# Optimization experiments

Measured on AMD Instinct MI355X. Metric: run time of the kernel, lower is better.

## Reference

```python
import jax, jax.numpy as jnp
import numpy as np

B = 4096
HASH_BITS = 128
TEACHER_DIM = 768
TEMPERATURE = 0.2
CONTRASTIVE_W = 1.0
DISTILL_W = 0.5
QUANT_W = 0.01


def _l2_normalize(x, eps=1e-12):
    # matches torch F.normalize(dim=-1)
    n = jnp.sqrt(jnp.sum(x * x, axis=-1, keepdims=True))
    return x / jnp.maximum(n, eps)


def setup_inputs() -> dict:
    key = jax.random.key(0)
    k1, k2, k3, k4 = jax.random.split(key, 4)
    logits = jax.random.normal(k1, (B, HASH_BITS), dtype=jnp.float32)
    # binary {-1,+1} codes as in the module contract
    hash_codes = jnp.sign(jax.random.normal(k2, (B, HASH_BITS), dtype=jnp.float32))
    hash_codes = jnp.where(hash_codes == 0, 1.0, hash_codes)
    teacher_embed = jax.random.normal(k3, (B, TEACHER_DIM), dtype=jnp.float32)
    # sparse random positives plus self-positives (guarantees each row nonempty)
    rand_pos = jax.random.uniform(k4, (B, B)) < 0.002
    eye = jnp.eye(B, dtype=bool)
    positive_mask = rand_pos | eye
    return {
        "logits": logits,
        "hash_codes": hash_codes,
        "teacher_embed": teacher_embed,
        "positive_mask": positive_mask,
    }


def reference(logits, hash_codes, teacher_embed, positive_mask):
    teacher = _l2_normalize(teacher_embed)

    # ---- contrastive (vectorized form of the per-row python loop) ----
    ln = _l2_normalize(logits)
    sim = (ln @ ln.T) / TEMPERATURE  # [B, B]
    eye = jnp.eye(sim.shape[0], dtype=bool)
    sim_masked = jnp.where(eye, -jnp.inf, sim)
    # per-row stable logsumexp over self-masked similarities
    log_denom = jax.nn.logsumexp(sim_masked, axis=1)  # [B]
    pm = positive_mask.astype(sim.dtype)
    cnt = pm.sum(axis=1)  # [B]
    pos_mean = (sim * pm).sum(axis=1) / jnp.maximum(cnt, 1.0)
    has_pos = cnt > 0
    per_row = jnp.where(has_pos, -pos_mean + log_denom, 0.0)
    num_pos = jnp.maximum(has_pos.sum(), 1)
    loss_cont = per_row.sum() / num_pos.astype(sim.dtype)

    # ---- distillation: hash similarity vs teacher similarity MSE ----
    hash_sim = (hash_codes @ hash_codes.T) / hash_codes.shape[-1]
    teacher_sim = teacher @ teacher.T
    loss_distill = jnp.mean((hash_sim - teacher_sim) ** 2)

    # ---- quantization: push |logits| toward 1 ----
    loss_quant = jnp.mean(jnp.abs(jnp.abs(logits) - 1.0))

    total = (
        CONTRASTIVE_W * loss_cont
        + DISTILL_W * loss_distill
        + QUANT_W * loss_quant
    )
    return total
```

## Files before the change

### kernel.cpp

```cpp
#include <hip/hip_runtime.h>


typedef __bf16 bf16x8 __attribute__((ext_vector_type(8)));
typedef float f32x4 __attribute__((ext_vector_type(4)));

__device__ __forceinline__ unsigned short f2bf(float f) {
  union { float f; unsigned int u; } v; v.f = f;
  unsigned int u = v.u;
  return (unsigned short)((u + 0x7FFFu + ((u >> 16) & 1u)) >> 16);
}

__global__ __launch_bounds__(256) void prep(const float* __restrict__ logits,
                                            const float* __restrict__ hash,
                                            const float* __restrict__ teacher,
                                            unsigned short* __restrict__ P,
                                            unsigned char* __restrict__ QT,
                                            float* __restrict__ qpart,
                                            float* __restrict__ rowexp,
                                            float* __restrict__ possum,
                                            float* __restrict__ cntw,
                                            float* __restrict__ dtot) {
  __shared__ float rnt[16];
  __shared__ unsigned char QL[16 * 897];
  const int t = threadIdx.x, wave = t >> 6, lane = t & 63;
  const int r0 = (int)blockIdx.x * 16;

#pragma unroll
  for (int rr = 0; rr < 4; ++rr) {
    const int rl = wave * 4 + rr, r = r0 + rl;
    float ss = 0.f;
#pragma unroll
    for (int i = 0; i < 12; ++i) {
      const float v = teacher[(size_t)r * 768 + i * 64 + lane];
      ss += v * v;
    }
    const float l0 = logits[(size_t)r * 128 + lane];
    const float l1 = logits[(size_t)r * 128 + 64 + lane];
    float ssl = l0 * l0 + l1 * l1;
    float qv = fabsf(fabsf(l0) - 1.f) + fabsf(fabsf(l1) - 1.f);
#pragma unroll
    for (int off = 1; off < 64; off <<= 1) {
      ss += __shfl_xor(ss, off, 64);
      ssl += __shfl_xor(ssl, off, 64);
      qv += __shfl_xor(qv, off, 64);
    }
    const float rnl = 1.f / fmaxf(sqrtf(ssl), 1e-12f);
    P[(size_t)r * 128 + lane] = f2bf(l0 * rnl);
    P[(size_t)r * 128 + 64 + lane] = f2bf(l1 * rnl);
    if (lane == 0) {
      rnt[rl] = 11.313708498984761f / fmaxf(sqrtf(ss), 1e-12f);
      qpart[r] = qv;
    }
  }
  if (t < 16) { rowexp[r0 + t] = 0.f; possum[r0 + t] = 0.f; cntw[r0 + t] = 0.f; }
  if (blockIdx.x == 0 && t == 0) *dtot = 0.f;
  __syncthreads();

#pragma unroll
  for (int it = 0; it < 4; ++it) {
    const int task = it * 256 + t;
    if (task < 896) {
      const int r = task / 56, cb = task % 56;
      const int r_g = r0 + r;
      unsigned char* dst = &QL[r * 897 + cb * 16];
      if (cb < 8) {
        const float4 v0 = *(const float4*)&hash[(size_t)r_g * 128 + cb * 16];
        const float4 v1 = *(const float4*)&hash[(size_t)r_g * 128 + cb * 16 + 4];
        const float4 v2 = *(const float4*)&hash[(size_t)r_g * 128 + cb * 16 + 8];
        const float4 v3 = *(const float4*)&hash[(size_t)r_g * 128 + cb * 16 + 12];
        const float vv[16] = {v0.x, v0.y, v0.z, v0.w, v1.x, v1.y, v1.z, v1.w,
                              v2.x, v2.y, v2.z, v2.w, v3.x, v3.y, v3.z, v3.w};
#pragma unroll
        for (int k = 0; k < 16; ++k) dst[k] = vv[k] >= 0.f ? 0x38 : 0xB8;
      } else {
        const float sc = rnt[r];
        const int c0 = cb * 16 - 128;
        const float4 v0 = *(const float4*)&teacher[(size_t)r_g * 768 + c0];
        const float4 v1 = *(const float4*)&teacher[(size_t)r_g * 768 + c0 + 4];
        const float4 v2 = *(const float4*)&teacher[(size_t)r_g * 768 + c0 + 8];
        const float4 v3 = *(const float4*)&teacher[(size_t)r_g * 768 + c0 + 12];
        const float vv[16] = {v0.x, v0.y, v0.z, v0.w, v1.x, v1.y, v1.z, v1.w,
                              v2.x, v2.y, v2.z, v2.w, v3.x, v3.y, v3.z, v3.w};
#pragma unroll
        for (int k = 0; k < 16; ++k) {
          const int p8 = __builtin_amdgcn_cvt_pk_fp8_f32(vv[k] * sc, vv[k] * sc,
                                                         0, false);
          dst[k] = (unsigned char)(p8 & 0xFF);
        }
      }
    }
  }
  __syncthreads();

#pragma unroll
  for (int i = 0; i < 4; ++i) {
    const int c = t + 256 * i;
    if (c < 896) {
      unsigned char buf[16];
#pragma unroll
      for (int j = 0; j < 16; ++j) buf[j] = QL[j * 897 + c];
      *(uint4*)&QT[(size_t)c * 4096 + r0] = *(uint4*)buf;
    }
  }
}

#define STAGE_GEN(GA, GB, PITCH)                                               \
  {                                                                            \
    _Pragma("unroll") for (int it = 0; it < 4; ++it) {                         \
      const int task = it * 256 + t;                                           \
      const int row = task >> 3;                                               \
      const int c16 = (task & 7) ^ (row & 7);                                  \
      const unsigned char* gpA = (GA) + (size_t)row * (PITCH) + c16 * 16;      \
      __builtin_amdgcn_global_load_lds(                                        \
          (const __attribute__((address_space(1))) void*)gpA,                  \
          (__attribute__((address_space(3))) void*)&SB[it * 4096 + wave * 1024],\
          16, 0, 0);                                                           \
      if (offdiag) {                                                           \
        const unsigned char* gpB = (GB) + (size_t)row * (PITCH) + c16 * 16;    \
        __builtin_amdgcn_global_load_lds(                                      \
            (const __attribute__((address_space(1))) void*)gpB,                \
            (__attribute__((address_space(3)))                                 \
                 void*)&SB[16384 + it * 4096 + wave * 1024],                   \
            16, 0, 0);                                                         \
      }                                                                        \
    }                                                                          \
  }

#define MFMA_B()                                                               \
  {                                                                            \
    _Pragma("unroll") for (int ks = 0; ks < 2; ++ks) {                         \
      const int ph = ((ks * 4 + qd) ^ (l15 & 7)) * 16;                         \
      bf16x8 af[4], bfr[4];                                                    \
      _Pragma("unroll") for (int rt = 0; rt < 4; ++rt)                         \
          af[rt] = *(const bf16x8*)&SB[(wy * 64 + rt * 16 + l15) * 128 + ph];  \
      _Pragma("unroll") for (int ct = 0; ct < 4; ++ct)                         \
          bfr[ct] = *(const bf16x8*)&SB[boffB +                                \
                                        (wx * 64 + ct * 16 + l15) * 128 + ph]; \
      _Pragma("unroll") for (int rt = 0; rt < 4; ++rt)                         \
          _Pragma("unroll") for (int ct = 0; ct < 4; ++ct) acc[rt][ct] =       \
          __builtin_amdgcn_mfma_f32_16x16x32_bf16(af[rt], bfr[ct],             \
                                                  acc[rt][ct], 0, 0, 0);       \
    }                                                                          \
  }

#define MFMA_Q()                                                               \
  {                                                                            \
    _Pragma("unroll") for (int ks = 0; ks < 4; ++ks) {                         \
      const int g0 = ks * 4 + qd;                                              \
      const int ph = ((g0 >> 1) ^ (l15 & 7)) * 16 + (g0 & 1) * 8;              \
      long af[4], bfr[4];                                                      \
      _Pragma("unroll") for (int rt = 0; rt < 4; ++rt)                         \
          af[rt] = *(const long*)&SB[(wy * 64 + rt * 16 + l15) * 128 + ph];    \
      _Pragma("unroll") for (int ct = 0; ct < 4; ++ct)                         \
          bfr[ct] = *(const long*)&SB[boffB +                                  \
                                      (wx * 64 + ct * 16 + l15) * 128 + ph];   \
      _Pragma("unroll") for (int rt = 0; rt < 4; ++rt)                         \
          _Pragma("unroll") for (int ct = 0; ct < 4; ++ct) acc[rt][ct] =       \
          __builtin_amdgcn_mfma_f32_16x16x32_fp8_fp8(af[rt], bfr[ct],          \
                                                     acc[rt][ct], 0, 0, 0);    \
    }                                                                          \
  }

__global__ __launch_bounds__(256, 3) void mega(const unsigned short* __restrict__ P,
                                               const unsigned char* __restrict__ QT,
                                               const void* __restrict__ mask,
                                               float* __restrict__ rowexp,
                                               float* __restrict__ possum,
                                               float* __restrict__ cntw,
                                               float* __restrict__ dtot) {
  __shared__ __align__(16) unsigned char SB[32768];
  __shared__ float redrow[128][2], red4[4];

  const int t = threadIdx.x;
  const int wave = t >> 6, lane = t & 63;
  const int qd = lane >> 4, l15 = lane & 15;
  const int wy = wave >> 1, wx = wave & 1;
  const int b = (int)blockIdx.x;

  f32x4 acc[4][4];
#pragma unroll
  for (int rt = 0; rt < 4; ++rt)
#pragma unroll
    for (int ct = 0; ct < 4; ++ct) acc[rt][ct] = {0.f, 0.f, 0.f, 0.f};

  if (b < 28) {
    int I = 0, rem = b;
    while (rem >= 7 - I) { rem -= 7 - I; ++I; }
    const int J = I + rem;
    const bool offdiag = (I != J);
    const int boffB = offdiag ? 16384 : 0;
    const unsigned char* QA = QT + (size_t)I * 128 * 4096;
    const unsigned char* QB = QT + (size_t)J * 128 * 4096;
    for (int kc = 0; kc < 32; ++kc) {
      __syncthreads();
      STAGE_GEN(QA + kc * 128, QB + kc * 128, 4096);
      __syncthreads();
      MFMA_Q();
    }
    float dsum = 0.f;
#pragma unroll
    for (int rt = 0; rt < 4; ++rt)
#pragma unroll
      for (int ct = 0; ct < 4; ++ct)
#pragma unroll
        for (int i = 0; i < 4; ++i) dsum += acc[rt][ct][i] * acc[rt][ct][i];
#pragma unroll
    for (int off = 1; off < 64; off <<= 1) dsum += __shfl_xor(dsum, off, 64);
    if (lane == 0) red4[wave] = dsum;
    __syncthreads();
    if (t == 0) {
      const float mult = (I == J ? 1.f : 2.f) *
                         (((I == 0) == (J == 0)) ? 1.f : -1.f);
      atomicAdd(dtot, mult * (red4[0] + red4[1] + red4[2] + red4[3]));
    }
  } else {
    const int bb = b - 28;
    const int l = (bb & 7) * 128 + (bb >> 3);
    const int bi = l >> 5, bj = l & 31;
    const int ti = bi * 128, tj = bj * 128;
    const bool offdiag = (bi != bj);
    const int boffB = offdiag ? 16384 : 0;

    const unsigned char* Pa = (const unsigned char*)(P + (size_t)ti * 128);
    const unsigned char* Pb = (const unsigned char*)(P + (size_t)tj * 128);
    for (int kc = 0; kc < 2; ++kc) {
      __syncthreads();
      STAGE_GEN(Pa + kc * 128, Pb + kc * 128, 256);
      __syncthreads();
      MFMA_B();
    }

    __syncthreads();
    unsigned char* MD = SB;
    const bool is_byte = ((const unsigned char*)mask)[4097] != 0;
    if (is_byte) {
      const unsigned char* m8d = (const unsigned char*)mask + (size_t)ti * 4096 + tj;
#pragma unroll
      for (int it = 0; it < 4; ++it) {
        const int task = it * 256 + t;
        const int row = task >> 3, seg = task & 7;
        __builtin_amdgcn_global_load_lds(
            (const __attribute__((address_space(1))) void*)
                (m8d + (size_t)row * 4096 + seg * 16),
            (__attribute__((address_space(3))) void*)&MD[it * 4096 + wave * 1024],
            16, 0, 0);
      }
    } else {
      const unsigned int* m32 = (const unsigned int*)mask;
#pragma unroll
      for (int it = 0; it < 16; ++it) {
        const int task = it * 256 + t;
        const int row = task >> 5, seg = task & 31;
        const uint4 v = *(const uint4*)&m32[(size_t)(ti + row) * 4096 + tj + seg * 4];
        uchar4 pk;
        pk.x = v.x ? 1 : 0; pk.y = v.y ? 1 : 0;
        pk.z = v.z ? 1 : 0; pk.w = v.w ? 1 : 0;
        *(uchar4*)&MD[row * 128 + seg * 4] = pk;
      }
    }
    __syncthreads();

#pragma unroll
    for (int rt = 0; rt < 4; ++rt) {
#pragma unroll
      for (int r = 0; r < 4; ++r) {
        const int mrow = wy * 64 + rt * 16 + qd * 4 + r;
        const int m = ti + mrow;
        float se = 0.f;
#pragma unroll
        for (int ct = 0; ct < 4; ++ct) {
          const int ncol = wx * 64 + ct * 16 + l15;
          const int n = tj + ncol;
          const float sim = acc[rt][ct][r] * 5.0f;
          const float e = __expf(sim);
          if (m != n) se += e;
          if (MD[mrow * 128 + ncol]) {
            atomicAdd(&possum[m], sim);
            atomicAdd(&cntw[m], 1.0f);
          }
        }
#pragma unroll
        for (int off = 1; off < 16; off <<= 1) se += __shfl_xor(se, off, 64);
        if (l15 == 0) redrow[mrow][wx] = se;
      }
    }
    __syncthreads();
    if (t < 128) atomicAdd(&rowexp[ti + t], redrow[t][0] + redrow[t][1]);
  }
}

__global__ __launch_bounds__(1024) void finalize(const float* __restrict__ rowexp,
                                                 const float* __restrict__ possum,
                                                 const float* __restrict__ cnt,
                                                 const float* __restrict__ qpart,
                                                 const float* __restrict__ dtot,
                                                 float* __restrict__ out) {
  const int t = threadIdx.x;
  const int wave = t >> 6, lane = t & 63;
  float c = 0.f, q = 0.f;
  for (int m = t; m < 4096; m += 1024) {
    c += logf(rowexp[m]) - possum[m] / fmaxf(cnt[m], 1.0f);
    q += qpart[m];
  }
#pragma unroll
  for (int off = 1; off < 64; off <<= 1) {
    c += __shfl_xor(c, off, 64);
    q += __shfl_xor(q, off, 64);
  }
  __shared__ float sc[16], sq[16];
  if (lane == 0) { sc[wave] = c; sq[wave] = q; }
  __syncthreads();
  if (t == 0) {
    float C = 0.f, Q = 0.f;
    for (int i = 0; i < 16; ++i) { C += sc[i]; Q += sq[i]; }
    out[0] = C * (1.0f / 4096.0f) + 0.5f * (dtot[0] * 3.6379788e-12f) +
             0.01f * (Q * (1.0f / 524288.0f));
  }
}

extern "C" void kernel_launch(void* const* d_in, const int* in_sizes, int n_in,
                              void* d_out, int out_size, void* d_ws, size_t ws_size,
                              hipStream_t stream) {
  const float* logits = (const float*)d_in[0];
  const float* hash = (const float*)d_in[1];
  const float* teacher = (const float*)d_in[2];
  const void* mask = d_in[3];
  float* out = (float*)d_out;

  char* ws = (char*)d_ws;
  float* rowexp = (float*)(ws + 0);
  float* possum = (float*)(ws + 16384);
  float* cntw = (float*)(ws + 32768);
  float* qpart = (float*)(ws + 49152);
  float* dtot = (float*)(ws + 65536);
  unsigned short* P = (unsigned short*)(ws + 98304);
  unsigned char* QT = (unsigned char*)(ws + 98304 + 1048576);

  prep<<<256, 256, 0, stream>>>(logits, hash, teacher, P, QT, qpart, rowexp,
                                possum, cntw, dtot);
  mega<<<1052, 256, 0, stream>>>(P, QT, mask, rowexp, possum, cntw, dtot);
  finalize<<<1, 1024, 0, stream>>>(rowexp, possum, cntw, qpart, dtot, out);
}
```

Measured before the change: 155.1 us.

## Drop LDS staging; load MFMA fragments directly from global with split-K distill tiles

Result: slower. 194.9 us (+25.7%).

```diff
diff --git a/kernel.cpp b/kernel.cpp
--- a/kernel.cpp
+++ b/kernel.cpp
@@ -104,63 +104,6 @@
   }
 }
 
-#define STAGE_GEN(GA, GB, PITCH)                                               \
-  {                                                                            \
-    _Pragma("unroll") for (int it = 0; it < 4; ++it) {                         \
-      const int task = it * 256 + t;                                           \
-      const int row = task >> 3;                                               \
-      const int c16 = (task & 7) ^ (row & 7);                                  \
-      const unsigned char* gpA = (GA) + (size_t)row * (PITCH) + c16 * 16;      \
-      __builtin_amdgcn_global_load_lds(                                        \
-          (const __attribute__((address_space(1))) void*)gpA,                  \
-          (__attribute__((address_space(3))) void*)&SB[it * 4096 + wave * 1024],\
-          16, 0, 0);                                                           \
-      if (offdiag) {                                                           \
-        const unsigned char* gpB = (GB) + (size_t)row * (PITCH) + c16 * 16;    \
-        __builtin_amdgcn_global_load_lds(                                      \
-            (const __attribute__((address_space(1))) void*)gpB,                \
-            (__attribute__((address_space(3)))                                 \
-                 void*)&SB[16384 + it * 4096 + wave * 1024],                   \
-            16, 0, 0);                                                         \
-      }                                                                        \
-    }                                                                          \
-  }
-
-#define MFMA_B()                                                               \
-  {                                                                            \
-    _Pragma("unroll") for (int ks = 0; ks < 2; ++ks) {                         \
-      const int ph = ((ks * 4 + qd) ^ (l15 & 7)) * 16;                         \
-      bf16x8 af[4], bfr[4];                                                    \
-      _Pragma("unroll") for (int rt = 0; rt < 4; ++rt)                         \
-          af[rt] = *(const bf16x8*)&SB[(wy * 64 + rt * 16 + l15) * 128 + ph];  \
-      _Pragma("unroll") for (int ct = 0; ct < 4; ++ct)                         \
-          bfr[ct] = *(const bf16x8*)&SB[boffB +                                \
-                                        (wx * 64 + ct * 16 + l15) * 128 + ph]; \
-      _Pragma("unroll") for (int rt = 0; rt < 4; ++rt)                         \
-          _Pragma("unroll") for (int ct = 0; ct < 4; ++ct) acc[rt][ct] =       \
-          __builtin_amdgcn_mfma_f32_16x16x32_bf16(af[rt], bfr[ct],             \
-                                                  acc[rt][ct], 0, 0, 0);       \
-    }                                                                          \
-  }
-
-#define MFMA_Q()                                                               \
-  {                                                                            \
-    _Pragma("unroll") for (int ks = 0; ks < 4; ++ks) {                         \
-      const int g0 = ks * 4 + qd;                                              \
-      const int ph = ((g0 >> 1) ^ (l15 & 7)) * 16 + (g0 & 1) * 8;              \
-      long af[4], bfr[4];                                                      \
-      _Pragma("unroll") for (int rt = 0; rt < 4; ++rt)                         \
-          af[rt] = *(const long*)&SB[(wy * 64 + rt * 16 + l15) * 128 + ph];    \
-      _Pragma("unroll") for (int ct = 0; ct < 4; ++ct)                         \
-          bfr[ct] = *(const long*)&SB[boffB +                                  \
-                                      (wx * 64 + ct * 16 + l15) * 128 + ph];   \
-      _Pragma("unroll") for (int rt = 0; rt < 4; ++rt)                         \
-          _Pragma("unroll") for (int ct = 0; ct < 4; ++ct) acc[rt][ct] =       \
-          __builtin_amdgcn_mfma_f32_16x16x32_fp8_fp8(af[rt], bfr[ct],          \
-                                                     acc[rt][ct], 0, 0, 0);    \
-    }                                                                          \
-  }
-
 __global__ __launch_bounds__(256, 3) void mega(const unsigned short* __restrict__ P,
                                                const unsigned char* __restrict__ QT,
                                                const void* __restrict__ mask,
@@ -168,13 +111,11 @@
                                                float* __restrict__ possum,
                                                float* __restrict__ cntw,
                                                float* __restrict__ dtot) {
-  __shared__ __align__(16) unsigned char SB[32768];
-  __shared__ float redrow[128][2], red4[4];
+  __shared__ float CD[3][64 * 65];
 
   const int t = threadIdx.x;
   const int wave = t >> 6, lane = t & 63;
   const int qd = lane >> 4, l15 = lane & 15;
-  const int wy = wave >> 1, wx = wave & 1;
   const int b = (int)blockIdx.x;
 
   f32x4 acc[4][4];
@@ -183,109 +124,112 @@
 #pragma unroll
     for (int ct = 0; ct < 4; ++ct) acc[rt][ct] = {0.f, 0.f, 0.f, 0.f};
 
-  if (b < 28) {
+  if (b < 105) {
     int I = 0, rem = b;
-    while (rem >= 7 - I) { rem -= 7 - I; ++I; }
+    while (rem >= 14 - I) { rem -= 14 - I; ++I; }
     const int J = I + rem;
-    const bool offdiag = (I != J);
-    const int boffB = offdiag ? 16384 : 0;
-    const unsigned char* QA = QT + (size_t)I * 128 * 4096;
-    const unsigned char* QB = QT + (size_t)J * 128 * 4096;
-    for (int kc = 0; kc < 32; ++kc) {
-      __syncthreads();
-      STAGE_GEN(QA + kc * 128, QB + kc * 128, 4096);
-      __syncthreads();
-      MFMA_Q();
-    }
-    float dsum = 0.f;
-#pragma unroll
-    for (int rt = 0; rt < 4; ++rt)
+    const unsigned char* Ab = QT + (size_t)(I * 64 + l15) * 4096 + wave * 1024 + qd * 8;
+    const unsigned char* Bb = QT + (size_t)(J * 64 + l15) * 4096 + wave * 1024 + qd * 8;
+#pragma unroll 4
+    for (int ks = 0; ks < 32; ++ks) {
+      long af[4], bfr[4];
+#pragma unroll
+      for (int rt = 0; rt < 4; ++rt)
+        af[rt] = *(const long*)(Ab + (size_t)rt * 16 * 4096 + ks * 32);
 #pragma unroll
       for (int ct = 0; ct < 4; ++ct)
-#pragma unroll
-        for (int i = 0; i < 4; ++i) dsum += acc[rt][ct][i] * acc[rt][ct][i];
-#pragma unroll
-    for (int off = 1; off < 64; off <<= 1) dsum += __shfl_xor(dsum, off, 64);
-    if (lane == 0) red4[wave] = dsum;
+        bfr[ct] = *(const long*)(Bb + (size_t)ct * 16 * 4096 + ks * 32);
+#pragma unroll
+      for (int rt = 0; rt < 4; ++rt)
+#pragma unroll
+        for (int ct = 0; ct < 4; ++ct)
+          acc[rt][ct] = __builtin_amdgcn_mfma_f32_16x16x32_fp8_fp8(
+              af[rt], bfr[ct], acc[rt][ct], 0, 0, 0);
+    }
+    if (wave != 0) {
+      float* dstl = &CD[wave - 1][lane * 65];
+#pragma unroll
+      for (int rt = 0; rt < 4; ++rt)
+#pragma unroll
+        for (int ct = 0; ct < 4; ++ct)
+#pragma unroll
+          for (int i = 0; i < 4; ++i)
+            dstl[rt * 16 + ct * 4 + i] = acc[rt][ct][i];
+    }
     __syncthreads();
-    if (t == 0) {
-      const float mult = (I == J ? 1.f : 2.f) *
-                         (((I == 0) == (J == 0)) ? 1.f : -1.f);
-      atomicAdd(dtot, mult * (red4[0] + red4[1] + red4[2] + red4[3]));
+    if (wave == 0) {
+      float dsum = 0.f;
+#pragma unroll
+      for (int rt = 0; rt < 4; ++rt)
+#pragma unroll
+        for (int ct = 0; ct < 4; ++ct)
+#pragma unroll
+          for (int i = 0; i < 4; ++i) {
+            const int idx = lane * 65 + rt * 16 + ct * 4 + i;
+            const float v = acc[rt][ct][i] + CD[0][idx] + CD[1][idx] + CD[2][idx];
+            dsum += v * v;
+          }
+#pragma unroll
+      for (int off = 1; off < 64; off <<= 1) dsum += __shfl_xor(dsum, off, 64);
+      if (lane == 0) {
+        const float mult = (I == J ? 1.f : 2.f) *
+                           (((I < 2) == (J < 2)) ? 1.f : -1.f);
+        atomicAdd(dtot, mult * dsum);
+      }
     }
   } else {
-    const int bb = b - 28;
+    const int bb = b - 105;
     const int l = (bb & 7) * 128 + (bb >> 3);
     const int bi = l >> 5, bj = l & 31;
     const int ti = bi * 128, tj = bj * 128;
-    const bool offdiag = (bi != bj);
-    const int boffB = offdiag ? 16384 : 0;
-
-    const unsigned char* Pa = (const unsigned char*)(P + (size_t)ti * 128);
-    const unsigned char* Pb = (const unsigned char*)(P + (size_t)tj * 128);
-    for (int kc = 0; kc < 2; ++kc) {
-      __syncthreads();
-      STAGE_GEN(Pa + kc * 128, Pb + kc * 128, 256);
-      __syncthreads();
-      MFMA_B();
-    }
-
-    __syncthreads();
-    unsigned char* MD = SB;
-    const bool is_byte = ((const unsigned char*)mask)[4097] != 0;
-    if (is_byte) {
-      const unsigned char* m8d = (const unsigned char*)mask + (size_t)ti * 4096 + tj;
-#pragma unroll
-      for (int it = 0; it < 4; ++it) {
-        const int task = it * 256 + t;
-        const int row = task >> 3, seg = task & 7;
-        __builtin_amdgcn_global_load_lds(
-            (const __attribute__((address_space(1))) void*)
-                (m8d + (size_t)row * 4096 + seg * 16),
-            (__attribute__((address_space(3))) void*)&MD[it * 4096 + wave * 1024],
-            16, 0, 0);
-      }
-    } else {
-      const unsigned int* m32 = (const unsigned int*)mask;
-#pragma unroll
-      for (int it = 0; it < 16; ++it) {
-        const int task = it * 256 + t;
-        const int row = task >> 5, seg = task & 31;
-        const uint4 v = *(const uint4*)&m32[(size_t)(ti + row) * 4096 + tj + seg * 4];
-        uchar4 pk;
-        pk.x = v.x ? 1 : 0; pk.y = v.y ? 1 : 0;
-        pk.z = v.z ? 1 : 0; pk.w = v.w ? 1 : 0;
-        *(uchar4*)&MD[row * 128 + seg * 4] = pk;
-      }
-    }
-    __syncthreads();
-
+    const int wy = wave >> 1, wx = wave & 1;
+
+    const unsigned short* Ab = P + (size_t)(ti + wy * 64 + l15) * 128 + qd * 8;
+    const unsigned short* Bb = P + (size_t)(tj + wx * 64 + l15) * 128 + qd * 8;
+#pragma unroll
+    for (int ks = 0; ks < 4; ++ks) {
+      bf16x8 af[4], bfr[4];
+#pragma unroll
+      for (int rt = 0; rt < 4; ++rt)
+        af[rt] = *(const bf16x8*)(Ab + rt * 16 * 128 + ks * 32);
+#pragma unroll
+      for (int ct = 0; ct < 4; ++ct)
+        bfr[ct] = *(const bf16x8*)(Bb + ct * 16 * 128 + ks * 32);
+#pragma unroll
+      for (int rt = 0; rt < 4; ++rt)
+#pragma unroll
+        for (int ct = 0; ct < 4; ++ct)
+          acc[rt][ct] = __builtin_amdgcn_mfma_f32_16x16x32_bf16(
+              af[rt], bfr[ct], acc[rt][ct], 0, 0, 0);
+    }
+
+    const unsigned char* m8 = (const unsigned char*)mask;
+    const unsigned int* m32 = (const unsigned int*)mask;
+    const bool is_byte = m8[4097] != 0;
 #pragma unroll
     for (int rt = 0; rt < 4; ++rt) {
 #pragma unroll
       for (int r = 0; r < 4; ++r) {
-        const int mrow = wy * 64 + rt * 16 + qd * 4 + r;
-        const int m = ti + mrow;
+        const int m = ti + wy * 64 + rt * 16 + qd * 4 + r;
         float se = 0.f;
 #pragma unroll
         for (int ct = 0; ct < 4; ++ct) {
-          const int ncol = wx * 64 + ct * 16 + l15;
-          const int n = tj + ncol;
+          const int n = tj + wx * 64 + ct * 16 + l15;
           const float sim = acc[rt][ct][r] * 5.0f;
           const float e = __expf(sim);
           if (m != n) se += e;
-          if (MD[mrow * 128 + ncol]) {
+          const bool pm = is_byte ? (m8[(size_t)m * 4096 + n] != 0)
+                                  : (m32[(size_t)m * 4096 + n] != 0);
+          if (pm) {
             atomicAdd(&possum[m], sim);
             atomicAdd(&cntw[m], 1.0f);
           }
         }
 #pragma unroll
         for (int off = 1; off < 16; off <<= 1) se += __shfl_xor(se, off, 64);
-        if (l15 == 0) redrow[mrow][wx] = se;
+        if (l15 == 0) atomicAdd(&rowexp[m], se);
       }
     }
-    __syncthreads();
-    if (t < 128) atomicAdd(&rowexp[ti + t], redrow[t][0] + redrow[t][1]);
   }
 }
 
@@ -338,6 +282,6 @@
 
   prep<<<256, 256, 0, stream>>>(logits, hash, teacher, P, QT, qpart, rowexp,
                                 possum, cntw, dtot);
-  mega<<<1052, 256, 0, stream>>>(P, QT, mask, rowexp, possum, cntw, dtot);
+  mega<<<1129, 256, 0, stream>>>(P, QT, mask, rowexp, possum, cntw, dtot);
   finalize<<<1, 1024, 0, stream>>>(rowexp, possum, cntw, qpart, dtot, out);
 }
```

## Exploit symmetry of contrastive similarity to compute only upper-triangular tiles

Applied to the files above, without the earlier changes.

After: 159.2 us. 1.03x slower.

```diff
diff --git a/kernel.cpp b/kernel.cpp
--- a/kernel.cpp
+++ b/kernel.cpp
@@ -169,7 +169,7 @@
                                                float* __restrict__ cntw,
                                                float* __restrict__ dtot) {
   __shared__ __align__(16) unsigned char SB[32768];
-  __shared__ float redrow[128][2], red4[4];
+  __shared__ float redrow[128][2], redcol[128][2], red4[4];
 
   const int t = threadIdx.x;
   const int wave = t >> 6, lane = t & 63;
@@ -215,8 +215,11 @@
     }
   } else {
     const int bb = b - 28;
-    const int l = (bb & 7) * 128 + (bb >> 3);
-    const int bi = l >> 5, bj = l & 31;
+    const int l = (bb & 7) * 66 + (bb >> 3);
+    int bi = (int)((65.0f - sqrtf(4225.0f - 8.0f * (float)l)) * 0.5f);
+    while (bi * (65 - bi) / 2 > l) --bi;
+    while ((bi + 1) * (64 - bi) / 2 <= l) ++bi;
+    const int bj = bi + (l - bi * (65 - bi) / 2);
     const int ti = bi * 128, tj = bj * 128;
     const bool offdiag = (bi != bj);
     const int boffB = offdiag ? 16384 : 0;
@@ -232,9 +235,11 @@
 
     __syncthreads();
     unsigned char* MD = SB;
+    unsigned char* MM = SB + 16384;
     const bool is_byte = ((const unsigned char*)mask)[4097] != 0;
     if (is_byte) {
       const unsigned char* m8d = (const unsigned char*)mask + (size_t)ti * 4096 + tj;
+      const unsigned char* m8m = (const unsigned char*)mask + (size_t)tj * 4096 + ti;
 #pragma unroll
       for (int it = 0; it < 4; ++it) {
         const int task = it * 256 + t;
@@ -244,6 +249,12 @@
                 (m8d + (size_t)row * 4096 + seg * 16),
             (__attribute__((address_space(3))) void*)&MD[it * 4096 + wave * 1024],
             16, 0, 0);
+        if (offdiag)
+          __builtin_amdgcn_global_load_lds(
+              (const __attribute__((address_space(1))) void*)
+                  (m8m + (size_t)row * 4096 + seg * 16),
+              (__attribute__((address_space(3))) void*)&MM[it * 4096 + wave * 1024],
+              16, 0, 0);
       }
     } else {
       const unsigned int* m32 = (const unsigned int*)mask;
@@ -256,10 +267,18 @@
         pk.x = v.x ? 1 : 0; pk.y = v.y ? 1 : 0;
         pk.z = v.z ? 1 : 0; pk.w = v.w ? 1 : 0;
         *(uchar4*)&MD[row * 128 + seg * 4] = pk;
+        if (offdiag) {
+          const uint4 w = *(const uint4*)&m32[(size_t)(tj + row) * 4096 + ti + seg * 4];
+          uchar4 pm;
+          pm.x = w.x ? 1 : 0; pm.y = w.y ? 1 : 0;
+          pm.z = w.z ? 1 : 0; pm.w = w.w ? 1 : 0;
+          *(uchar4*)&MM[row * 128 + seg * 4] = pm;
+        }
       }
     }
     __syncthreads();
 
+    float colp[4] = {0.f, 0.f, 0.f, 0.f};
 #pragma unroll
     for (int rt = 0; rt < 4; ++rt) {
 #pragma unroll
@@ -273,19 +292,36 @@
           const int n = tj + ncol;
           const float sim = acc[rt][ct][r] * 5.0f;
           const float e = __expf(sim);
-          if (m != n) se += e;
+          if (offdiag || mrow != ncol) se += e;
+          if (offdiag) colp[ct] += e;
           if (MD[mrow * 128 + ncol]) {
             atomicAdd(&possum[m], sim);
             atomicAdd(&cntw[m], 1.0f);
           }
+          if (offdiag && MM[ncol * 128 + mrow]) {
+            atomicAdd(&possum[n], sim);
+            atomicAdd(&cntw[n], 1.0f);
+          }
         }
 #pragma unroll
         for (int off = 1; off < 16; off <<= 1) se += __shfl_xor(se, off, 64);
         if (l15 == 0) redrow[mrow][wx] = se;
       }
     }
+    if (offdiag) {
+#pragma unroll
+      for (int ct = 0; ct < 4; ++ct) {
+        float ce = colp[ct];
+        ce += __shfl_xor(ce, 16, 64);
+        ce += __shfl_xor(ce, 32, 64);
+        if (qd == 0) redcol[wx * 64 + ct * 16 + l15][wy] = ce;
+      }
+    }
     __syncthreads();
-    if (t < 128) atomicAdd(&rowexp[ti + t], redrow[t][0] + redrow[t][1]);
+    if (t < 128) {
+      atomicAdd(&rowexp[ti + t], redrow[t][0] + redrow[t][1]);
+      if (offdiag) atomicAdd(&rowexp[tj + t], redcol[t][0] + redcol[t][1]);
+    }
   }
 }
 
@@ -338,6 +374,6 @@
 
   prep<<<256, 256, 0, stream>>>(logits, hash, teacher, P, QT, qpart, rowexp,
                                 possum, cntw, dtot);
-  mega<<<1052, 256, 0, stream>>>(P, QT, mask, rowexp, possum, cntw, dtot);
+  mega<<<556, 256, 0, stream>>>(P, QT, mask, rowexp, possum, cntw, dtot);
   finalize<<<1, 1024, 0, stream>>>(rowexp, possum, cntw, qpart, dtot, out);
 }
```

## Quantize normalized logits to FP8 and run contrastive GEMM with FP8 MFMA

Applied to the files above, without the earlier changes.

Result: no change. 155.8 us (+0.4%).

```diff
diff --git a/kernel.cpp b/kernel.cpp
--- a/kernel.cpp
+++ b/kernel.cpp
@@ -1,19 +1,12 @@
 #include <hip/hip_runtime.h>
 
 
-typedef __bf16 bf16x8 __attribute__((ext_vector_type(8)));
 typedef float f32x4 __attribute__((ext_vector_type(4)));
-
-__device__ __forceinline__ unsigned short f2bf(float f) {
-  union { float f; unsigned int u; } v; v.f = f;
-  unsigned int u = v.u;
-  return (unsigned short)((u + 0x7FFFu + ((u >> 16) & 1u)) >> 16);
-}
 
 __global__ __launch_bounds__(256) void prep(const float* __restrict__ logits,
                                             const float* __restrict__ hash,
                                             const float* __restrict__ teacher,
-                                            unsigned short* __restrict__ P,
+                                            unsigned char* __restrict__ Pq,
                                             unsigned char* __restrict__ QT,
                                             float* __restrict__ qpart,
                                             float* __restrict__ rowexp,
@@ -34,10 +27,9 @@
       const float v = teacher[(size_t)r * 768 + i * 64 + lane];
       ss += v * v;
     }
-    const float l0 = logits[(size_t)r * 128 + lane];
-    const float l1 = logits[(size_t)r * 128 + 64 + lane];
-    float ssl = l0 * l0 + l1 * l1;
-    float qv = fabsf(fabsf(l0) - 1.f) + fabsf(fabsf(l1) - 1.f);
+    const float2 lv = *(const float2*)&logits[(size_t)r * 128 + 2 * lane];
+    float ssl = lv.x * lv.x + lv.y * lv.y;
+    float qv = fabsf(fabsf(lv.x) - 1.f) + fabsf(fabsf(lv.y) - 1.f);
 #pragma unroll
     for (int off = 1; off < 64; off <<= 1) {
       ss += __shfl_xor(ss, off, 64);
@@ -45,8 +37,8 @@
       qv += __shfl_xor(qv, off, 64);
     }
     const float rnl = 1.f / fmaxf(sqrtf(ssl), 1e-12f);
-    P[(size_t)r * 128 + lane] = f2bf(l0 * rnl);
-    P[(size_t)r * 128 + 64 + lane] = f2bf(l1 * rnl);
+    const int p8 = __builtin_amdgcn_cvt_pk_fp8_f32(lv.x * rnl, lv.y * rnl, 0, false);
+    *(unsigned short*)&Pq[(size_t)r * 128 + 2 * lane] = (unsigned short)(p8 & 0xFFFF);
     if (lane == 0) {
       rnt[rl] = 11.313708498984761f / fmaxf(sqrtf(ss), 1e-12f);
       qpart[r] = qv;
@@ -126,23 +118,6 @@
     }                                                                          \
   }
 
-#define MFMA_B()                                                               \
-  {                                                                            \
-    _Pragma("unroll") for (int ks = 0; ks < 2; ++ks) {                         \
-      const int ph = ((ks * 4 + qd) ^ (l15 & 7)) * 16;                         \
-      bf16x8 af[4], bfr[4];                                                    \
-      _Pragma("unroll") for (int rt = 0; rt < 4; ++rt)                         \
-          af[rt] = *(const bf16x8*)&SB[(wy * 64 + rt * 16 + l15) * 128 + ph];  \
-      _Pragma("unroll") for (int ct = 0; ct < 4; ++ct)                         \
-          bfr[ct] = *(const bf16x8*)&SB[boffB +                                \
-                                        (wx * 64 + ct * 16 + l15) * 128 + ph]; \
-      _Pragma("unroll") for (int rt = 0; rt < 4; ++rt)                         \
-          _Pragma("unroll") for (int ct = 0; ct < 4; ++ct) acc[rt][ct] =       \
-          __builtin_amdgcn_mfma_f32_16x16x32_bf16(af[rt], bfr[ct],             \
-                                                  acc[rt][ct], 0, 0, 0);       \
-    }                                                                          \
-  }
-
 #define MFMA_Q()                                                               \
   {                                                                            \
     _Pragma("unroll") for (int ks = 0; ks < 4; ++ks) {                         \
@@ -161,14 +136,14 @@
     }                                                                          \
   }
 
-__global__ __launch_bounds__(256, 3) void mega(const unsigned short* __restrict__ P,
+__global__ __launch_bounds__(256, 3) void mega(const unsigned char* __restrict__ Pq,
                                                const unsigned char* __restrict__ QT,
                                                const void* __restrict__ mask,
                                                float* __restrict__ rowexp,
                                                float* __restrict__ possum,
                                                float* __restrict__ cntw,
                                                float* __restrict__ dtot) {
-  __shared__ __align__(16) unsigned char SB[32768];
+  __shared__ __align__(16) unsigned char SB[49152];
   __shared__ float redrow[128][2], red4[4];
 
   const int t = threadIdx.x;
@@ -221,17 +196,8 @@
     const bool offdiag = (bi != bj);
     const int boffB = offdiag ? 16384 : 0;
 
-    const unsigned char* Pa = (const unsigned char*)(P + (size_t)ti * 128);
-    const unsigned char* Pb = (const unsigned char*)(P + (size_t)tj * 128);
-    for (int kc = 0; kc < 2; ++kc) {
-      __syncthreads();
-      STAGE_GEN(Pa + kc * 128, Pb + kc * 128, 256);
-      __syncthreads();
-      MFMA_B();
-    }
-
-    __syncthreads();
-    unsigned char* MD = SB;
+    STAGE_GEN(Pq + (size_t)ti * 128, Pq + (size_t)tj * 128, 128);
+    unsigned char* MD = SB + 32768;
     const bool is_byte = ((const unsigned char*)mask)[4097] != 0;
     if (is_byte) {
       const unsigned char* m8d = (const unsigned char*)mask + (size_t)ti * 4096 + tj;
@@ -259,6 +225,8 @@
       }
     }
     __syncthreads();
+
+    MFMA_Q();
 
 #pragma unroll
     for (int rt = 0; rt < 4; ++rt) {
@@ -333,11 +301,11 @@
   float* cntw = (float*)(ws + 32768);
   float* qpart = (float*)(ws + 49152);
   float* dtot = (float*)(ws + 65536);
-  unsigned short* P = (unsigned short*)(ws + 98304);
+  unsigned char* Pq = (unsigned char*)(ws + 98304);
   unsigned char* QT = (unsigned char*)(ws + 98304 + 1048576);
 
-  prep<<<256, 256, 0, stream>>>(logits, hash, teacher, P, QT, qpart, rowexp,
+  prep<<<256, 256, 0, stream>>>(logits, hash, teacher, Pq, QT, qpart, rowexp,
                                 possum, cntw, dtot);
-  mega<<<1052, 256, 0, stream>>>(P, QT, mask, rowexp, possum, cntw, dtot);
+  mega<<<1052, 256, 0, stream>>>(Pq, QT, mask, rowexp, possum, cntw, dtot);
   finalize<<<1, 1024, 0, stream>>>(rowexp, possum, cntw, qpart, dtot, out);
 }
```
